# Optimization experiments

Measured on AMD Instinct MI355X. Metric: run time of the kernel, lower is better.

Reference implementation:

```python
import jax, jax.numpy as jnp
import numpy as np

B, N, H, NH = 2, 2048, 1024, 16
HD = H // NH


def setup_inputs() -> dict:
    key = jax.random.key(0)
    ks = jax.random.split(key, 12)
    s = 0.02
    inp = {
        "q": jax.random.normal(ks[0], (B, N, H), jnp.float32),
        "k": jax.random.normal(ks[1], (B, N, H), jnp.float32),
        "v": jax.random.normal(ks[2], (B, N, H), jnp.float32),
        # causal mask, broadcast over batch and heads
        "mask": jnp.tril(jnp.ones((N, N), jnp.float32))[None, None, :, :],
        "Wq": jax.random.normal(ks[3], (H, H), jnp.float32) * s,
        "bq": jnp.zeros((H,), jnp.float32),
        "Wk": jax.random.normal(ks[4], (H, H), jnp.float32) * s,
        "bk": jnp.zeros((H,), jnp.float32),
        "Wv": jax.random.normal(ks[5], (H, H), jnp.float32) * s,
        "bv": jnp.zeros((H,), jnp.float32),
        "Wp": jax.random.normal(ks[6], (H, H), jnp.float32) * s,
        "bp": jnp.zeros((H,), jnp.float32),
    }
    return inp


def _split_heads(x):
    # [b, n, (h d)] -> [b, h, n, d]
    b, n, _ = x.shape
    return x.reshape(b, n, NH, HD).transpose(0, 2, 1, 3)


def reference(q, k, v, mask, Wq, bq, Wk, bk, Wv, bv, Wp, bp):
    Q = _split_heads(q @ Wq.T + bq)                      # [b,h,n,d]
    K = _split_heads(k @ Wk.T + bk)
    V = _split_heads(v @ Wv.T + bv)
    scores = jnp.einsum("bhnd,bhmd->bhnm", Q, K) / jnp.sqrt(jnp.float32(HD))
    scores = jnp.where(mask == 0, -jnp.inf, scores)
    attn = jax.nn.softmax(scores, axis=-1)
    out = jnp.einsum("bhnm,bhmd->bhnd", attn, V)         # [b,h,n,d]
    out = out.transpose(0, 2, 1, 3).reshape(q.shape[0], q.shape[1], H)
    # dropout is identity in eval mode
    return out @ Wp.T + bp
```

## Files before the change

kernel.cpp:

```cpp
#include <hip/hip_runtime.h>


typedef unsigned short ushortT;
typedef unsigned int uintT;
typedef __attribute__((ext_vector_type(8))) short short8;
typedef __attribute__((ext_vector_type(4))) float f32x4;

#define M_ROWS 4096
#define KDIM   1024
#define NDIM   1024
#define SEQ    2048
#define HDHEAD 64

__device__ __forceinline__ float bf2f(ushortT s) {
    union { unsigned u; float f; } v; v.u = ((unsigned)s) << 16; return v.f;
}
__device__ __forceinline__ ushortT f2bf(float x) {
    union { float f; unsigned u; } v; v.f = x;
    return (ushortT)((v.u + 0x7fffu + ((v.u >> 16) & 1u)) >> 16);
}

__device__ __forceinline__ bool detect_f32(const uintT* w) {
    int hits = 0;
#pragma unroll
    for (int i = 0; i < 16; ++i) {
        const unsigned e = (w[i] >> 7) & 0xffu;
        hits += (e >= 118u && e <= 131u) ? 1 : 0;
    }
    return hits < 8;
}

__device__ __forceinline__ short8 cvt8(const float* p) {
    f32x4 a = *(const f32x4*)p;
    f32x4 b = *(const f32x4*)(p + 4);
    short8 r;
    r[0] = (short)f2bf(a[0]); r[1] = (short)f2bf(a[1]);
    r[2] = (short)f2bf(a[2]); r[3] = (short)f2bf(a[3]);
    r[4] = (short)f2bf(b[0]); r[5] = (short)f2bf(b[1]);
    r[6] = (short)f2bf(b[2]); r[7] = (short)f2bf(b[3]);
    return r;
}

__device__ __forceinline__ void gl2lds16(const ushortT* g, ushortT* l) {
    __builtin_amdgcn_global_load_lds(
        (const __attribute__((address_space(1))) void*)g,
        (__attribute__((address_space(3))) void*)l,
        16, 0, 0);
}

__global__ __launch_bounds__(256) void convert_kernel(
    const void* __restrict__ q, const void* __restrict__ k, const void* __restrict__ v,
    const void* __restrict__ Wq, const void* __restrict__ Wk,
    const void* __restrict__ Wv, const void* __restrict__ Wp,
    const void* __restrict__ bq, const void* __restrict__ bk,
    const void* __restrict__ bv, const void* __restrict__ bp,
    ushortT* __restrict__ dst) {
    const bool f32m = detect_f32((const uintT*)q);
    const size_t u = (size_t)blockIdx.x * 256 + threadIdx.x;

    const void* src; size_t soff, doff;
    if (u < 1572864u) {
        const int seg = (int)(u >> 19);
        const size_t o = u & 524287u;
        src  = seg == 0 ? q : (seg == 1 ? k : v);
        soff = o * 8;
        doff = (size_t)seg * 4194304u + o * 8;
    } else if (u < 2097152u) {
        const size_t u2 = u - 1572864u;
        const int seg = (int)(u2 >> 17);
        const size_t o = u2 & 131071u;
        src  = seg == 0 ? Wq : (seg == 1 ? Wk : (seg == 2 ? Wv : Wp));
        soff = o * 8;
        doff = 12582912u + (size_t)seg * 1048576u + o * 8;
    } else {
        const size_t u3 = u - 2097152u;
        const int seg = (int)(u3 >> 7);
        const size_t o = u3 & 127u;
        src  = seg == 0 ? bq : (seg == 1 ? bk : (seg == 2 ? bv : bp));
        soff = o * 8;
        doff = 16777216u + (size_t)seg * 1024u + o * 8;
    }

    if (f32m)
        *(short8*)(dst + doff) = cvt8((const float*)src + soff);
    else
        *(short8*)(dst + doff) = *(const short8*)((const ushortT*)src + soff);
}

__device__ __forceinline__ void gemm_body(const void* __restrict__ Av,
                                          const void* __restrict__ Wv_,
                                          const void* __restrict__ biasv,
                                          void* __restrict__ Cv,
                                          bool a_f32, bool w_f32, bool c_f32,
                                          float cscale, bool vt_store) {
    __shared__ ushortT ldsA[128 * 64];
    __shared__ ushortT ldsB[128 * 64];

    const int tid  = threadIdx.x;
    const int lane = tid & 63;
    const int wid  = tid >> 6;
    const int bm   = blockIdx.x;
    const int bn   = blockIdx.y;
    const int wm   = wid >> 1;
    const int wn   = wid & 1;

    const int srow = lane >> 2;
    const int scol = (lane & 3) * 8;

    f32x4 acc[4][4];
#pragma unroll
    for (int i = 0; i < 4; ++i)
#pragma unroll
        for (int j = 0; j < 4; ++j) acc[i][j] = (f32x4){0.f, 0.f, 0.f, 0.f};

    const int fr   = lane & 15;
    const int quad = lane >> 4;

    for (int kt = 0; kt < KDIM / 64; ++kt) {
        const int k0 = kt * 64;
        if (!a_f32 && !w_f32) {
#pragma unroll
            for (int t = 0; t < 4; ++t) {
                const int chunk = wid * 4 + t;
                const int kh  = chunk >> 3;
                const int r16 = (chunk & 7) * 16;
                const size_t ra = (size_t)(bm * 128 + r16 + srow) * KDIM + k0 + kh * 32 + scol;
                const size_t rw = (size_t)(bn * 128 + r16 + srow) * KDIM + k0 + kh * 32 + scol;
                gl2lds16((const ushortT*)Av + ra, ldsA + chunk * 512);
                gl2lds16((const ushortT*)Wv_ + rw, ldsB + chunk * 512);
            }
        } else {
            short8 ta[4], tb[4];
#pragma unroll
            for (int t = 0; t < 4; ++t) {
                const int chunk = wid * 4 + t;
                const int kh  = chunk >> 3;
                const int r16 = (chunk & 7) * 16;
                const size_t ra = (size_t)(bm * 128 + r16 + srow) * KDIM + k0 + kh * 32 + scol;
                const size_t rw = (size_t)(bn * 128 + r16 + srow) * KDIM + k0 + kh * 32 + scol;
                ta[t] = a_f32 ? cvt8((const float*)Av + ra)
                              : *(const short8*)((const ushortT*)Av + ra);
                tb[t] = w_f32 ? cvt8((const float*)Wv_ + rw)
                              : *(const short8*)((const ushortT*)Wv_ + rw);
            }
#pragma unroll
            for (int t = 0; t < 4; ++t) {
                const int chunk = wid * 4 + t;
                *(short8*)(ldsA + chunk * 512 + lane * 8) = ta[t];
                *(short8*)(ldsB + chunk * 512 + lane * 8) = tb[t];
            }
        }
        __syncthreads();

#pragma unroll
        for (int s = 0; s < 2; ++s) {
            short8 aF[4], bF[4];
#pragma unroll
            for (int i = 0; i < 4; ++i)
                aF[i] = *(const short8*)(ldsA + s * 4096 + (wm * 64 + i * 16 + fr) * 32 + quad * 8);
#pragma unroll
            for (int j = 0; j < 4; ++j)
                bF[j] = *(const short8*)(ldsB + s * 4096 + (wn * 64 + j * 16 + fr) * 32 + quad * 8);
#pragma unroll
            for (int i = 0; i < 4; ++i)
#pragma unroll
                for (int j = 0; j < 4; ++j)
                    acc[i][j] = __builtin_amdgcn_mfma_f32_16x16x32_bf16(aF[i], bF[j], acc[i][j], 0, 0, 0);
        }
        __syncthreads();
    }

#pragma unroll
    for (int j = 0; j < 4; ++j) {
        const int col = bn * 128 + wn * 64 + j * 16 + fr;
        const float bv = w_f32 ? ((const float*)biasv)[col]
                               : bf2f(((const ushortT*)biasv)[col]);
#pragma unroll
        for (int i = 0; i < 4; ++i) {
            const int row0 = bm * 128 + wm * 64 + i * 16 + quad * 4;
#pragma unroll
            for (int r = 0; r < 4; ++r) {
                const float val = (acc[i][j][r] + bv) * cscale;
                const int row = row0 + r;
                if (vt_store) {
                    const int bb = row >> 11, n = row & 2047;
                    const int hh = col >> 6,  d = col & 63;
                    ((ushortT*)Cv)[(size_t)((bb * 16 + hh) * 64 + d) * SEQ + n] = f2bf(val);
                } else if (c_f32) {
                    ((float*)Cv)[(size_t)row * NDIM + col] = val;
                } else {
                    ((ushortT*)Cv)[(size_t)row * NDIM + col] = f2bf(val);
                }
            }
        }
    }
}

__global__ __launch_bounds__(256, 2) void qkv_proj_kernel(
    const void* __restrict__ q, const void* __restrict__ k, const void* __restrict__ v,
    const void* __restrict__ Wq, const void* __restrict__ Wk, const void* __restrict__ Wv,
    const void* __restrict__ bq, const void* __restrict__ bk, const void* __restrict__ bv,
    ushortT* __restrict__ Qp, ushortT* __restrict__ Kp, ushortT* __restrict__ Vt) {
    const bool f32m = detect_f32((const uintT*)q);
    const void* A; const void* W; const void* bias; ushortT* C;
    float cscale = 1.f; bool vt = false;
    if (blockIdx.z == 0)      { A = q; W = Wq; bias = bq; C = Qp; cscale = 0.125f; }
    else if (blockIdx.z == 1) { A = k; W = Wk; bias = bk; C = Kp; }
    else                      { A = v; W = Wv; bias = bv; C = Vt; vt = true; }
    gemm_body(A, W, bias, (void*)C, f32m, f32m, false, cscale, vt);
}

__global__ __launch_bounds__(256, 2) void out_proj_kernel(
    const ushortT* __restrict__ A, const void* __restrict__ W,
    const void* __restrict__ bias, void* __restrict__ C,
    const void* __restrict__ qdet) {
    const bool wf = detect_f32((const uintT*)W);
    const bool cf = detect_f32((const uintT*)qdet);
    gemm_body((const void*)A, W, bias, C, false, wf, cf, 1.f, false);
}

__global__ __launch_bounds__(256, 2) void flash_attn_kernel(
    const ushortT* __restrict__ Qp, const ushortT* __restrict__ Kp,
    const ushortT* __restrict__ Vt, ushortT* __restrict__ Op) {
    __shared__ ushortT ldsK[2 * 64 * 40];
    __shared__ ushortT ldsV[64 * 72];
    __shared__ ushortT ldsP[4][16 * 72];

    const int tid  = threadIdx.x;
    const int lane = tid & 63;
    const int wid  = tid >> 6;
    const int fr   = lane & 15;
    const int quad = lane >> 4;

    const int lin = blockIdx.x;
    const int xcd = lin & 7;
    const int j   = lin >> 3;
    const int bh  = xcd * 4 + (j & 3);
    const int pid = j >> 2;
    const int h   = bh & 15;
    const int b   = bh >> 4;

    const size_t base  = (size_t)b * SEQ * NDIM + (size_t)h * HDHEAD;
    const size_t vtb   = (size_t)(b * 16 + h) * HDHEAD * SEQ;

    int ksst[2], keyloc[2];
#pragma unroll
    for (int t = 0; t < 2; ++t) {
        const int chunk = wid * 2 + t;
        ksst[t]   = chunk >> 2;
        keyloc[t] = (chunk & 3) * 16 + (lane >> 2);
    }
    const int c8 = (lane & 3) * 8;
    const int vd  = lane >> 3;
    const int vk8 = (lane & 7) * 8;

    for (int half = 0; half < 2; ++half) {
        const int qb = (half == 0) ? pid : (31 - pid);
        const int q0 = qb * 64;
        const int nkv = qb + 1;

        short8 qf[2];
#pragma unroll
        for (int ks = 0; ks < 2; ++ks)
            qf[ks] = *(const short8*)(Qp + base + (size_t)(q0 + wid * 16 + fr) * NDIM + ks * 32 + quad * 8);

        f32x4 accO[4];
#pragma unroll
        for (int dt = 0; dt < 4; ++dt) accO[dt] = (f32x4){0.f, 0.f, 0.f, 0.f};
        float lsum[4];
#pragma unroll
        for (int r = 0; r < 4; ++r) lsum[r] = 0.f;

        short8 kreg[2], vreg[2];
#pragma unroll
        for (int t = 0; t < 2; ++t) {
            kreg[t] = *(const short8*)(Kp + base + (size_t)keyloc[t] * NDIM + ksst[t] * 32 + c8);
            const int d = (wid * 2 + t) * 8 + vd;
            vreg[t] = *(const short8*)(Vt + vtb + (size_t)d * SEQ + vk8);
        }

        for (int kt = 0; kt < nkv; ++kt) {
            __syncthreads();

#pragma unroll
            for (int t = 0; t < 2; ++t) {
                *(short8*)(ldsK + ksst[t] * 2560 + keyloc[t] * 40 + c8) = kreg[t];
                const int d = (wid * 2 + t) * 8 + vd;
                *(short8*)(ldsV + d * 72 + vk8) = vreg[t];
            }

            if (kt + 1 < nkv) {
                const int kv1 = (kt + 1) * 64;
#pragma unroll
                for (int t = 0; t < 2; ++t) {
                    kreg[t] = *(const short8*)(Kp + base + (size_t)(kv1 + keyloc[t]) * NDIM + ksst[t] * 32 + c8);
                    const int d = (wid * 2 + t) * 8 + vd;
                    vreg[t] = *(const short8*)(Vt + vtb + (size_t)d * SEQ + kv1 + vk8);
                }
            }
            __syncthreads();

            f32x4 s[4];
#pragma unroll
            for (int nt = 0; nt < 4; ++nt) {
                f32x4 a = (f32x4){0.f, 0.f, 0.f, 0.f};
#pragma unroll
                for (int ks = 0; ks < 2; ++ks) {
                    short8 kf = *(const short8*)(ldsK + ks * 2560 + (nt * 16 + fr) * 40 + quad * 8);
                    a = __builtin_amdgcn_mfma_f32_16x16x32_bf16(qf[ks], kf, a, 0, 0, 0);
                }
                s[nt] = a;
            }

            const int kv0 = kt * 64;
            const int qi = q0 + wid * 16 + quad * 4;
            if (kt == nkv - 1) {
#pragma unroll
                for (int nt = 0; nt < 4; ++nt) {
                    const int kj = kv0 + nt * 16 + fr;
#pragma unroll
                    for (int r = 0; r < 4; ++r)
                        s[nt][r] = (kj > qi + r) ? -1e30f : s[nt][r];
                }
            }

            ushortT* pbuf = ldsP[wid];
#pragma unroll
            for (int nt = 0; nt < 4; ++nt) {
#pragma unroll
                for (int r = 0; r < 4; ++r) {
                    const float p = __expf(fminf(s[nt][r], 30.f));
                    lsum[r] += p;
                    pbuf[(quad * 4 + r) * 72 + nt * 16 + fr] = f2bf(p);
                }
            }

            asm volatile("" ::: "memory");

#pragma unroll
            for (int ks = 0; ks < 2; ++ks) {
                short8 pf = *(const short8*)(pbuf + fr * 72 + ks * 32 + quad * 8);
#pragma unroll
                for (int dt = 0; dt < 4; ++dt) {
                    short8 vf = *(const short8*)(ldsV + (dt * 16 + fr) * 72 + ks * 32 + quad * 8);
                    accO[dt] = __builtin_amdgcn_mfma_f32_16x16x32_bf16(pf, vf, accO[dt], 0, 0, 0);
                }
            }
        }

#pragma unroll
        for (int r = 0; r < 4; ++r) {
#pragma unroll
            for (int off = 8; off >= 1; off >>= 1)
                lsum[r] += __shfl_xor(lsum[r], off, 64);
        }
#pragma unroll
        for (int dt = 0; dt < 4; ++dt) {
#pragma unroll
            for (int r = 0; r < 4; ++r) {
                const size_t row = (size_t)(q0 + wid * 16 + quad * 4 + r);
                Op[(size_t)b * SEQ * NDIM + row * NDIM + h * HDHEAD + dt * 16 + fr] =
                    f2bf(accO[dt][r] / lsum[r]);
            }
        }
    }
}

extern "C" void kernel_launch(void* const* d_in, const int* in_sizes, int n_in,
                              void* d_out, int out_size, void* d_ws, size_t ws_size,
                              hipStream_t stream) {
    const void* q  = d_in[0];
    const void* k  = d_in[1];
    const void* v  = d_in[2];
    const void* Wq = d_in[4];
    const void* bq = d_in[5];
    const void* Wk = d_in[6];
    const void* bk = d_in[7];
    const void* Wv = d_in[8];
    const void* bv = d_in[9];
    const void* Wp = d_in[10];
    const void* bp = d_in[11];

    dim3 blk(256);
    const size_t FAST_WS = 58728448;

    if (ws_size >= FAST_WS) {
        ushortT* cb   = (ushortT*)d_ws;
        ushortT* qb16 = cb;
        ushortT* kb16 = cb + 4194304u;
        ushortT* vb16 = cb + 8388608u;
        ushortT* Wqb  = cb + 12582912u;
        ushortT* Wkb  = cb + 13631488u;
        ushortT* Wvb  = cb + 14680064u;
        ushortT* Wpb  = cb + 15728640u;
        ushortT* bqb  = cb + 16777216u;
        ushortT* bkb  = cb + 16778240u;
        ushortT* bvb  = cb + 16779264u;
        ushortT* bpb  = cb + 16780288u;
        ushortT* Qp   = cb + 16781312u;
        ushortT* Kp   = Qp + 4194304u;
        ushortT* Vt   = Kp + 4194304u;
        ushortT* Op   = qb16;

        convert_kernel<<<dim3(8194), blk, 0, stream>>>(
            q, k, v, Wq, Wk, Wv, Wp, bq, bk, bv, bp, cb);
        qkv_proj_kernel<<<dim3(32, 8, 3), blk, 0, stream>>>(
            qb16, kb16, vb16, Wqb, Wkb, Wvb, bqb, bkb, bvb, Qp, Kp, Vt);
        flash_attn_kernel<<<dim3(512), blk, 0, stream>>>(Qp, Kp, Vt, Op);
        out_proj_kernel<<<dim3(32, 8), blk, 0, stream>>>(Op, Wpb, bpb, d_out, q);
    } else {
        ushortT* ws = (ushortT*)d_ws;
        ushortT* Qp = ws;
        ushortT* Kp = ws + (size_t)M_ROWS * NDIM;
        ushortT* Vt = ws + (size_t)2 * M_ROWS * NDIM;
        ushortT* Op = ws + (size_t)3 * M_ROWS * NDIM;

        qkv_proj_kernel<<<dim3(32, 8, 3), blk, 0, stream>>>(
            q, k, v, Wq, Wk, Wv, bq, bk, bv, Qp, Kp, Vt);
        flash_attn_kernel<<<dim3(512), blk, 0, stream>>>(Qp, Kp, Vt, Op);
        out_proj_kernel<<<dim3(32, 8), blk, 0, stream>>>(Op, Wp, bp, d_out, q);
    }
}
```

Measured before the change: 236.0 us.

## Process paired causal query blocks together sharing K/V tile loads

Each flash-attention block now processes both query blocks of a causal pair (pid and 31-pid) in one pass over the key/value tiles. Each K/V tile is loaded into LDS once and reused by both query blocks, with the short block masked off after its diagonal. This removes the repeated K/V loads for the shorter block. The block-to-work mapping is also changed to interleave pids across blocks. The cost is doubled accumulator and P-buffer state, which raises register and LDS pressure and may hurt occupancy under launch_bounds(256,2).

```diff
diff --git a/kernel.cpp b/kernel.cpp
--- a/kernel.cpp
+++ b/kernel.cpp
@@ -224,7 +224,8 @@
     const ushortT* __restrict__ Vt, ushortT* __restrict__ Op) {
     __shared__ ushortT ldsK[2 * 64 * 40];
     __shared__ ushortT ldsV[64 * 72];
-    __shared__ ushortT ldsP[4][16 * 72];
+    __shared__ ushortT ldsP0[4][16 * 72];
+    __shared__ ushortT ldsP1[4][16 * 72];
 
     const int tid  = threadIdx.x;
     const int lane = tid & 63;
@@ -233,10 +234,11 @@
     const int quad = lane >> 4;
 
     const int lin = blockIdx.x;
-    const int xcd = lin & 7;
-    const int j   = lin >> 3;
-    const int bh  = xcd * 4 + (j & 3);
-    const int pid = j >> 2;
+    const int c   = lin & 255;
+    const int g   = lin >> 8;
+    const int bh  = c & 31;
+    const int t   = c >> 5;
+    const int pid = g ? (15 - t) : t;
     const int h   = bh & 15;
     const int b   = bh >> 4;
 
@@ -245,123 +247,169 @@
 
     int ksst[2], keyloc[2];
 #pragma unroll
-    for (int t = 0; t < 2; ++t) {
-        const int chunk = wid * 2 + t;
-        ksst[t]   = chunk >> 2;
-        keyloc[t] = (chunk & 3) * 16 + (lane >> 2);
+    for (int u = 0; u < 2; ++u) {
+        const int chunk = wid * 2 + u;
+        ksst[u]   = chunk >> 2;
+        keyloc[u] = (chunk & 3) * 16 + (lane >> 2);
     }
     const int c8 = (lane & 3) * 8;
     const int vd  = lane >> 3;
     const int vk8 = (lane & 7) * 8;
 
-    for (int half = 0; half < 2; ++half) {
-        const int qb = (half == 0) ? pid : (31 - pid);
-        const int q0 = qb * 64;
-        const int nkv = qb + 1;
-
-        short8 qf[2];
-#pragma unroll
-        for (int ks = 0; ks < 2; ++ks)
-            qf[ks] = *(const short8*)(Qp + base + (size_t)(q0 + wid * 16 + fr) * NDIM + ks * 32 + quad * 8);
-
-        f32x4 accO[4];
-#pragma unroll
-        for (int dt = 0; dt < 4; ++dt) accO[dt] = (f32x4){0.f, 0.f, 0.f, 0.f};
-        float lsum[4];
-#pragma unroll
-        for (int r = 0; r < 4; ++r) lsum[r] = 0.f;
-
-        short8 kreg[2], vreg[2];
-#pragma unroll
-        for (int t = 0; t < 2; ++t) {
-            kreg[t] = *(const short8*)(Kp + base + (size_t)keyloc[t] * NDIM + ksst[t] * 32 + c8);
-            const int d = (wid * 2 + t) * 8 + vd;
-            vreg[t] = *(const short8*)(Vt + vtb + (size_t)d * SEQ + vk8);
-        }
-
-        for (int kt = 0; kt < nkv; ++kt) {
-            __syncthreads();
-
-#pragma unroll
-            for (int t = 0; t < 2; ++t) {
-                *(short8*)(ldsK + ksst[t] * 2560 + keyloc[t] * 40 + c8) = kreg[t];
-                const int d = (wid * 2 + t) * 8 + vd;
-                *(short8*)(ldsV + d * 72 + vk8) = vreg[t];
-            }
-
-            if (kt + 1 < nkv) {
-                const int kv1 = (kt + 1) * 64;
-#pragma unroll
-                for (int t = 0; t < 2; ++t) {
-                    kreg[t] = *(const short8*)(Kp + base + (size_t)(kv1 + keyloc[t]) * NDIM + ksst[t] * 32 + c8);
-                    const int d = (wid * 2 + t) * 8 + vd;
-                    vreg[t] = *(const short8*)(Vt + vtb + (size_t)d * SEQ + kv1 + vk8);
+    const int q00 = pid * 64;
+    const int q01 = (31 - pid) * 64;
+    const int nkv = 32 - pid;
+
+    short8 qf0[2], qf1[2];
+#pragma unroll
+    for (int ks = 0; ks < 2; ++ks) {
+        qf0[ks] = *(const short8*)(Qp + base + (size_t)(q00 + wid * 16 + fr) * NDIM + ks * 32 + quad * 8);
+        qf1[ks] = *(const short8*)(Qp + base + (size_t)(q01 + wid * 16 + fr) * NDIM + ks * 32 + quad * 8);
+    }
+
+    f32x4 accO0[4], accO1[4];
+#pragma unroll
+    for (int dt = 0; dt < 4; ++dt) {
+        accO0[dt] = (f32x4){0.f, 0.f, 0.f, 0.f};
+        accO1[dt] = (f32x4){0.f, 0.f, 0.f, 0.f};
+    }
+    float lsum0[4], lsum1[4];
+#pragma unroll
+    for (int r = 0; r < 4; ++r) { lsum0[r] = 0.f; lsum1[r] = 0.f; }
+
+    short8 kreg[2], vreg[2];
+#pragma unroll
+    for (int u = 0; u < 2; ++u) {
+        kreg[u] = *(const short8*)(Kp + base + (size_t)keyloc[u] * NDIM + ksst[u] * 32 + c8);
+        const int d = (wid * 2 + u) * 8 + vd;
+        vreg[u] = *(const short8*)(Vt + vtb + (size_t)d * SEQ + vk8);
+    }
+
+    const int qi0 = q00 + wid * 16 + quad * 4;
+    const int qi1 = q01 + wid * 16 + quad * 4;
+
+    for (int kt = 0; kt < nkv; ++kt) {
+        __syncthreads();
+
+#pragma unroll
+        for (int u = 0; u < 2; ++u) {
+            *(short8*)(ldsK + ksst[u] * 2560 + keyloc[u] * 40 + c8) = kreg[u];
+            const int d = (wid * 2 + u) * 8 + vd;
+            *(short8*)(ldsV + d * 72 + vk8) = vreg[u];
+        }
+
+        if (kt + 1 < nkv) {
+            const int kv1 = (kt + 1) * 64;
+#pragma unroll
+            for (int u = 0; u < 2; ++u) {
+                kreg[u] = *(const short8*)(Kp + base + (size_t)(kv1 + keyloc[u]) * NDIM + ksst[u] * 32 + c8);
+                const int d = (wid * 2 + u) * 8 + vd;
+                vreg[u] = *(const short8*)(Vt + vtb + (size_t)d * SEQ + kv1 + vk8);
+            }
+        }
+        __syncthreads();
+
+        const bool act0 = (kt <= pid);
+
+        f32x4 s0[4], s1[4];
+#pragma unroll
+        for (int nt = 0; nt < 4; ++nt) {
+            short8 kf[2];
+#pragma unroll
+            for (int ks = 0; ks < 2; ++ks)
+                kf[ks] = *(const short8*)(ldsK + ks * 2560 + (nt * 16 + fr) * 40 + quad * 8);
+            f32x4 a1 = (f32x4){0.f, 0.f, 0.f, 0.f};
+#pragma unroll
+            for (int ks = 0; ks < 2; ++ks)
+                a1 = __builtin_amdgcn_mfma_f32_16x16x32_bf16(qf1[ks], kf[ks], a1, 0, 0, 0);
+            s1[nt] = a1;
+            if (act0) {
+                f32x4 a0 = (f32x4){0.f, 0.f, 0.f, 0.f};
+#pragma unroll
+                for (int ks = 0; ks < 2; ++ks)
+                    a0 = __builtin_amdgcn_mfma_f32_16x16x32_bf16(qf0[ks], kf[ks], a0, 0, 0, 0);
+                s0[nt] = a0;
+            }
+        }
+
+        const int kv0 = kt * 64;
+        if (kt == nkv - 1) {
+#pragma unroll
+            for (int nt = 0; nt < 4; ++nt) {
+                const int kj = kv0 + nt * 16 + fr;
+#pragma unroll
+                for (int r = 0; r < 4; ++r)
+                    s1[nt][r] = (kj > qi1 + r) ? -1e30f : s1[nt][r];
+            }
+        }
+        if (act0 && kt == pid) {
+#pragma unroll
+            for (int nt = 0; nt < 4; ++nt) {
+                const int kj = kv0 + nt * 16 + fr;
+#pragma unroll
+                for (int r = 0; r < 4; ++r)
+                    s0[nt][r] = (kj > qi0 + r) ? -1e30f : s0[nt][r];
+            }
+        }
+
+        ushortT* pbuf1 = ldsP1[wid];
+#pragma unroll
+        for (int nt = 0; nt < 4; ++nt) {
+#pragma unroll
+            for (int r = 0; r < 4; ++r) {
+                const float p = __expf(fminf(s1[nt][r], 30.f));
+                lsum1[r] += p;
+                pbuf1[(quad * 4 + r) * 72 + nt * 16 + fr] = f2bf(p);
+            }
+        }
+        ushortT* pbuf0 = ldsP0[wid];
+        if (act0) {
+#pragma unroll
+            for (int nt = 0; nt < 4; ++nt) {
+#pragma unroll
+                for (int r = 0; r < 4; ++r) {
+                    const float p = __expf(fminf(s0[nt][r], 30.f));
+                    lsum0[r] += p;
+                    pbuf0[(quad * 4 + r) * 72 + nt * 16 + fr] = f2bf(p);
                 }
             }
-            __syncthreads();
-
-            f32x4 s[4];
-#pragma unroll
-            for (int nt = 0; nt < 4; ++nt) {
-                f32x4 a = (f32x4){0.f, 0.f, 0.f, 0.f};
-#pragma unroll
-                for (int ks = 0; ks < 2; ++ks) {
-                    short8 kf = *(const short8*)(ldsK + ks * 2560 + (nt * 16 + fr) * 40 + quad * 8);
-                    a = __builtin_amdgcn_mfma_f32_16x16x32_bf16(qf[ks], kf, a, 0, 0, 0);
-                }
-                s[nt] = a;
-            }
-
-            const int kv0 = kt * 64;
-            const int qi = q0 + wid * 16 + quad * 4;
-            if (kt == nkv - 1) {
-#pragma unroll
-                for (int nt = 0; nt < 4; ++nt) {
-                    const int kj = kv0 + nt * 16 + fr;
-#pragma unroll
-                    for (int r = 0; r < 4; ++r)
-                        s[nt][r] = (kj > qi + r) ? -1e30f : s[nt][r];
-                }
-            }
-
-            ushortT* pbuf = ldsP[wid];
-#pragma unroll
-            for (int nt = 0; nt < 4; ++nt) {
-#pragma unroll
-                for (int r = 0; r < 4; ++r) {
-                    const float p = __expf(fminf(s[nt][r], 30.f));
-                    lsum[r] += p;
-                    pbuf[(quad * 4 + r) * 72 + nt * 16 + fr] = f2bf(p);
-                }
-            }
-
-            asm volatile("" ::: "memory");
-
-#pragma unroll
-            for (int ks = 0; ks < 2; ++ks) {
-                short8 pf = *(const short8*)(pbuf + fr * 72 + ks * 32 + quad * 8);
-#pragma unroll
-                for (int dt = 0; dt < 4; ++dt) {
-                    short8 vf = *(const short8*)(ldsV + (dt * 16 + fr) * 72 + ks * 32 + quad * 8);
-                    accO[dt] = __builtin_amdgcn_mfma_f32_16x16x32_bf16(pf, vf, accO[dt], 0, 0, 0);
-                }
-            }
-        }
-
+        }
+
+        asm volatile("" ::: "memory");
+
+#pragma unroll
+        for (int ks = 0; ks < 2; ++ks) {
+            short8 pf1 = *(const short8*)(pbuf1 + fr * 72 + ks * 32 + quad * 8);
+            short8 pf0;
+            if (act0) pf0 = *(const short8*)(pbuf0 + fr * 72 + ks * 32 + quad * 8);
+#pragma unroll
+            for (int dt = 0; dt < 4; ++dt) {
+                short8 vf = *(const short8*)(ldsV + (dt * 16 + fr) * 72 + ks * 32 + quad * 8);
+                accO1[dt] = __builtin_amdgcn_mfma_f32_16x16x32_bf16(pf1, vf, accO1[dt], 0, 0, 0);
+                if (act0)
+                    accO0[dt] = __builtin_amdgcn_mfma_f32_16x16x32_bf16(pf0, vf, accO0[dt], 0, 0, 0);
+            }
+        }
+    }
+
+#pragma unroll
+    for (int r = 0; r < 4; ++r) {
+#pragma unroll
+        for (int off = 8; off >= 1; off >>= 1) {
+            lsum0[r] += __shfl_xor(lsum0[r], off, 64);
+            lsum1[r] += __shfl_xor(lsum1[r], off, 64);
+        }
+    }
+#pragma unroll
+    for (int dt = 0; dt < 4; ++dt) {
 #pragma unroll
         for (int r = 0; r < 4; ++r) {
-#pragma unroll
-            for (int off = 8; off >= 1; off >>= 1)
-                lsum[r] += __shfl_xor(lsum[r], off, 64);
-        }
-#pragma unroll
-        for (int dt = 0; dt < 4; ++dt) {
-#pragma unroll
-            for (int r = 0; r < 4; ++r) {
-                const size_t row = (size_t)(q0 + wid * 16 + quad * 4 + r);
-                Op[(size_t)b * SEQ * NDIM + row * NDIM + h * HDHEAD + dt * 16 + fr] =
-                    f2bf(accO[dt][r] / lsum[r]);
-            }
+            const size_t row0 = (size_t)(q00 + wid * 16 + quad * 4 + r);
+            const size_t row1 = (size_t)(q01 + wid * 16 + quad * 4 + r);
+            Op[(size_t)b * SEQ * NDIM + row0 * NDIM + h * HDHEAD + dt * 16 + fr] =
+                f2bf(accO0[dt][r] / lsum0[r]);
+            Op[(size_t)b * SEQ * NDIM + row1 * NDIM + h * HDHEAD + dt * 16 + fr] =
+                f2bf(accO1[dt][r] / lsum1[r]);
         }
     }
 }
```

Measured after the change: 237.9 us. No clear change (+0.8%).
